# Kernel tuning notes

Hardware: AMD Instinct MI355X
Metric: run time of the kernel (lower is better)

## Reference

```python
import jax, jax.numpy as jnp
import numpy as np

SEQ = 8192
D_IN = 1024
D_OUT = 128


def setup_inputs() -> dict:
    key = jax.random.key(0)
    k0, k1, k2, k3 = jax.random.split(key, 4)
    # kaiming-normal-ish init for weights (std = sqrt(2/fan_in))
    std = np.sqrt(2.0 / D_IN).astype(np.float32)
    return {
        "x": jax.random.normal(k0, (SEQ, D_IN), dtype=jnp.float32),
        "wq": jax.random.normal(k1, (D_IN, D_OUT), dtype=jnp.float32) * std,
        "wk": jax.random.normal(k2, (D_IN, D_OUT), dtype=jnp.float32) * std,
        "wv": jax.random.normal(k3, (D_IN, D_OUT), dtype=jnp.float32) * std,
    }


def reference(x, wq, wk, wv):
    # q,k,v: [S, d_out]
    q = x @ wq
    k = x @ wk
    v = x @ wv
    scale = jnp.sqrt(jnp.asarray(D_OUT, dtype=q.dtype))
    scores = (q @ k.T) / scale          # [S, S]
    attn = jax.nn.softmax(scores, axis=-1)
    return attn @ v                      # [S, d_out]
```

## Files before the change

kernel.cpp:

```cpp
#include <hip/hip_runtime.h>
#include <cstdint>

#define SEQ    8192
#define DIN    1024
#define DOUT   128
#define NSPLIT 8
#define KVTILE 64
#define QTILE  128
#define QK_SCALE 0.1275174246f
#define RESCALE_THR 8.0f

typedef unsigned short u16;
typedef __bf16 bf16x8 __attribute__((ext_vector_type(8)));
typedef float  f32x4  __attribute__((ext_vector_type(4)));
typedef float  f32x16 __attribute__((ext_vector_type(16)));
typedef unsigned short u16x8 __attribute__((ext_vector_type(8)));
typedef unsigned short u16x4 __attribute__((ext_vector_type(4)));

__device__ __forceinline__ u16 bfc(float f) {
  return __builtin_bit_cast(u16, (__bf16)f);
}
__device__ __forceinline__ float bf2f(u16 u) {
  union { uint32_t u; float f; } c; c.u = ((uint32_t)u) << 16; return c.f;
}

__device__ __forceinline__ bf16x8 ldsu8(const u16* base, int byteoff) {
  return __builtin_bit_cast(bf16x8,
    *reinterpret_cast<const u16x8*>(reinterpret_cast<const char*>(base) + byteoff));
}
__device__ __forceinline__ bf16x8 glbu8(const u16* p) {
  return __builtin_bit_cast(bf16x8, *reinterpret_cast<const u16x8*>(p));
}

__device__ __forceinline__ void gload_lds16(const void* g, void* l) {
  __builtin_amdgcn_global_load_lds(
      (const __attribute__((address_space(1))) void*)g,
      (__attribute__((address_space(3))) void*)l, 16, 0, 0);
}

__global__ __launch_bounds__(256) void k_wtrans(const float* __restrict__ wq,
                                                const float* __restrict__ wk,
                                                const float* __restrict__ wv,
                                                u16* __restrict__ Wt) {
  const float* w = (blockIdx.y == 0) ? wq : (blockIdx.y == 1) ? wk : wv;
  int idx = blockIdx.x * 256 + threadIdx.x;
  int k = idx >> 7, n = idx & 127;
  Wt[(size_t)blockIdx.y * (DOUT * DIN) + (size_t)n * DIN + k] = bfc(w[idx]);
}

__global__ __launch_bounds__(256) void k_xcast(const float* __restrict__ x,
                                               u16* __restrict__ Xb) {
  size_t base = ((size_t)blockIdx.x * 256 + threadIdx.x) * 8;
  float4 lo = *reinterpret_cast<const float4*>(x + base);
  float4 hi = *reinterpret_cast<const float4*>(x + base + 4);
  u16x8 v = { bfc(lo.x), bfc(lo.y), bfc(lo.z), bfc(lo.w),
              bfc(hi.x), bfc(hi.y), bfc(hi.z), bfc(hi.w) };
  *reinterpret_cast<u16x8*>(Xb + base) = v;
}

__global__ __launch_bounds__(256, 2) void k_gemm(const u16* __restrict__ Xb,
                                                 const u16* __restrict__ Wt,
                                                 u16* __restrict__ Q,
                                                 u16* __restrict__ K,
                                                 u16* __restrict__ Vt) {
  __shared__ __attribute__((aligned(16))) u16 As[2][64 * 128];
  __shared__ __attribute__((aligned(16))) u16 Bs[2][96 * 128];
  const int tid  = threadIdx.x;
  const int lane = tid & 63, wave = tid >> 6;
  const int lm   = lane & 15, g = lane >> 4;
  const int wm   = wave >> 1, wn = wave & 1;
  const int m0   = blockIdx.x * 64;
  const int n0   = blockIdx.y * 96;
  const int swzr = (lm & 7) << 4;

  const int trow = tid >> 4;
  const int tswz = ((tid & 15) << 4) ^ ((trow & 7) << 4);
  const char* baseA = (const char*)Xb + (size_t)(m0 + trow) * 2048 + tswz;
  const char* baseB = (const char*)Wt + (size_t)(n0 + trow) * 2048 + tswz;

  auto stage = [&](int buf, int kc) {
    const int kb = kc * 256;
#pragma unroll
    for (int i = 0; i < 4; ++i)
      gload_lds16(baseA + kb + i * 32768, &As[buf][i * 2048 + wave * 512]);
#pragma unroll
    for (int j = 0; j < 6; ++j)
      gload_lds16(baseB + kb + j * 32768, &Bs[buf][j * 2048 + wave * 512]);
  };

  f32x4 acc[2][3];
#pragma unroll
  for (int s = 0; s < 2; ++s)
#pragma unroll
    for (int nb = 0; nb < 3; ++nb) acc[s][nb] = (f32x4){0.f, 0.f, 0.f, 0.f};

  auto compute = [&](int buf) {
    const u16* As_ = As[buf];
    const u16* Bs_ = Bs[buf];
    bf16x8 a[2][4], b[3][4];
#pragma unroll
    for (int s = 0; s < 2; ++s)
#pragma unroll
      for (int t = 0; t < 4; ++t)
        a[s][t] = ldsu8(As_, (wm * 32 + s * 16 + lm) * 256 +
                             ((t * 64 + 16 * g) ^ swzr));
#pragma unroll
    for (int nb = 0; nb < 3; ++nb)
#pragma unroll
      for (int t = 0; t < 4; ++t)
        b[nb][t] = ldsu8(Bs_, (wn * 48 + nb * 16 + lm) * 256 +
                              ((t * 64 + 16 * g) ^ swzr));
#pragma unroll
    for (int s = 0; s < 2; ++s)
#pragma unroll
      for (int nb = 0; nb < 3; ++nb)
#pragma unroll
        for (int t = 0; t < 4; ++t)
          acc[s][nb] = __builtin_amdgcn_mfma_f32_16x16x32_bf16(
              a[s][t], b[nb][t], acc[s][nb], 0, 0, 0);
  };

  stage(0, 0);
  asm volatile("s_waitcnt vmcnt(0)" ::: "memory");
  __syncthreads();

#pragma unroll
  for (int kc = 0; kc < 8; kc += 2) {
    if (kc + 1 < 8) stage(1, kc + 1);
    compute(0);
    asm volatile("s_waitcnt vmcnt(0)" ::: "memory");
    __syncthreads();
    if (kc + 2 < 8) stage(0, kc + 2);
    compute(1);
    asm volatile("s_waitcnt vmcnt(0)" ::: "memory");
    __syncthreads();
  }

#pragma unroll
  for (int s = 0; s < 2; ++s)
#pragma unroll
    for (int nb = 0; nb < 3; ++nb) {
      int n = n0 + wn * 48 + nb * 16 + lm;
      int which = n >> 7, col = n & 127;
#pragma unroll
      for (int r = 0; r < 4; ++r) {
        int m = m0 + wm * 32 + s * 16 + g * 4 + r;
        if (which == 0)       Q[(size_t)m * DOUT + col] = bfc(acc[s][nb][r] * QK_SCALE);
        else if (which == 1)  K[(size_t)m * DOUT + col] = bfc(acc[s][nb][r]);
        else                  Vt[(size_t)col * SEQ + m] = bfc(acc[s][nb][r]);
      }
    }
}

__global__ __launch_bounds__(256, 2) void k_attn(const u16* __restrict__ Q,
                                                 const u16* __restrict__ K,
                                                 const u16* __restrict__ Vt,
                                                 u16* __restrict__ Op,
                                                 float* __restrict__ Mb,
                                                 float* __restrict__ Lb) {
  __shared__ __attribute__((aligned(16))) u16 Ks[2][64 * 128];
  __shared__ __attribute__((aligned(16))) u16 Vts[2][128 * 64];
  __shared__ __attribute__((aligned(16))) u16 Ps[4][32 * 64];
  const int tid  = threadIdx.x;
  const int lane = tid & 63, wave = tid >> 6;
  const int l31  = lane & 31, h = lane >> 5;
  const int bid  = blockIdx.x;
  const int split = bid & 7;
  const int m0   = (bid >> 3) * QTILE;
  const int kvbase = split * (SEQ / NSPLIT);
  const int NIT = (SEQ / NSPLIT) / KVTILE;

  auto stage = [&](int buf, int kv0) {
#pragma unroll
    for (int i = 0; i < 4; ++i) {
      int krow = wave * 16 + i * 4 + (lane >> 4);
      const char* gk = (const char*)K + ((size_t)(kv0 + krow) << 8) +
                       (((lane & 15) << 4) ^ ((krow & 7) << 4));
      gload_lds16(gk, &Ks[buf][wave * 2048 + i * 512]);
      int vrow = wave * 32 + i * 8 + (lane >> 3);
      const char* gv = (const char*)Vt + (size_t)vrow * (SEQ * 2) +
                       (size_t)kv0 * 2 +
                       (((lane & 7) << 4) ^ ((vrow & 7) << 4));
      gload_lds16(gv, &Vts[buf][wave * 2048 + i * 512]);
    }
  };

  bf16x8 qf[8];
  stage(0, kvbase);
  {
    const u16* qp = Q + (size_t)(m0 + wave * 32 + l31) * DOUT + 8 * h;
#pragma unroll
    for (int t = 0; t < 8; ++t) qf[t] = glbu8(qp + t * 16);
  }
  asm volatile("s_waitcnt vmcnt(0)" ::: "memory");
  __syncthreads();

  f32x16 o[4] = {};
  float mr = -1e30f, lr = 0.f;

  u16* pw = Ps[wave];
  char* pwb = reinterpret_cast<char*>(pw) + l31 * 128;
  const int pswz = (l31 & 7) << 4;
  int cur = 0;

  for (int it = 0; it < NIT; ++it) {
    if (it + 1 < NIT) stage(cur ^ 1, kvbase + (it + 1) * KVTILE);

    const u16* ks = Ks[cur];
    const u16* vs = Vts[cur];

    f32x16 s[2];
    __builtin_amdgcn_s_setprio(1);
#pragma unroll
    for (int kb = 0; kb < 2; ++kb) {
      f32x16 a = {};
      int krow = kb * 32 + l31;
      int rswz = (krow & 7) << 4;
#pragma unroll
      for (int t = 0; t < 8; ++t) {
        bf16x8 kf = ldsu8(ks, krow * 256 + ((t * 32 + 16 * h) ^ rswz));
        a = __builtin_amdgcn_mfma_f32_32x32x16_bf16(kf, qf[t], a, 0, 0, 0);
      }
      s[kb] = a;
    }
    __builtin_amdgcn_s_setprio(0);

    float t8[8];
#pragma unroll
    for (int i = 0; i < 8; ++i)
      t8[i] = fmaxf(fmaxf(s[0][2 * i], s[0][2 * i + 1]),
                    fmaxf(s[1][2 * i], s[1][2 * i + 1]));
    float u0 = fmaxf(fmaxf(t8[0], t8[1]), fmaxf(t8[2], t8[3]));
    float u1 = fmaxf(fmaxf(t8[4], t8[5]), fmaxf(t8[6], t8[7]));
    float rm = fmaxf(u0, u1);
    rm = fmaxf(rm, __shfl_xor(rm, 32));

    if (__any(rm - mr > RESCALE_THR)) {
      float mn = fmaxf(mr, rm);
      float alpha = exp2f(mr - mn);
      mr = mn;
      lr *= alpha;
#pragma unroll
      for (int db = 0; db < 4; ++db) o[db] *= alpha;
    }

    float rsum = 0.f;
#pragma unroll
    for (int kb = 0; kb < 2; ++kb)
#pragma unroll
      for (int j = 0; j < 4; ++j) {
        float p0 = exp2f(s[kb][4 * j + 0] - mr);
        float p1 = exp2f(s[kb][4 * j + 1] - mr);
        float p2 = exp2f(s[kb][4 * j + 2] - mr);
        float p3 = exp2f(s[kb][4 * j + 3] - mr);
        u16x4 w = { bfc(p0), bfc(p1), bfc(p2), bfc(p3) };
        *reinterpret_cast<u16x4*>(pwb +
            ((kb * 64 + 16 * j + 8 * h) ^ pswz)) = w;
        rsum += (p0 + p1) + (p2 + p3);
      }
    lr += rsum;

    asm volatile("s_waitcnt lgkmcnt(0)" ::: "memory");
    __builtin_amdgcn_sched_barrier(0);

    __builtin_amdgcn_s_setprio(1);
#pragma unroll
    for (int j = 0; j < 4; ++j) {
      bf16x8 pb = ldsu8(pw, l31 * 128 + ((32 * j + 16 * h) ^ pswz));
#pragma unroll
      for (int db = 0; db < 4; ++db) {
        int vrow = db * 32 + l31;
        bf16x8 vb = ldsu8(vs, vrow * 128 +
                              ((32 * j + 16 * h) ^ ((vrow & 7) << 4)));
        o[db] = __builtin_amdgcn_mfma_f32_32x32x16_bf16(vb, pb, o[db], 0, 0, 0);
      }
    }
    __builtin_amdgcn_s_setprio(0);

    asm volatile("s_waitcnt vmcnt(0)" ::: "memory");
    __syncthreads();
    cur ^= 1;
  }

  lr += __shfl_xor(lr, 32);

  const size_t ob = (size_t)split * SEQ * DOUT;
  const int q = m0 + wave * 32 + l31;
#pragma unroll
  for (int db = 0; db < 4; ++db)
#pragma unroll
    for (int j = 0; j < 4; ++j) {
      u16x4 w = { bfc(o[db][4 * j + 0]), bfc(o[db][4 * j + 1]),
                  bfc(o[db][4 * j + 2]), bfc(o[db][4 * j + 3]) };
      *reinterpret_cast<u16x4*>(Op + ob + (size_t)q * DOUT +
                                db * 32 + 8 * j + 4 * h) = w;
    }
  if (h == 0) {
    Mb[split * SEQ + q] = mr;
    Lb[split * SEQ + q] = lr;
  }
}

__global__ __launch_bounds__(256) void k_combine(const u16* __restrict__ Op,
                                                 const float* __restrict__ Mb,
                                                 const float* __restrict__ Lb,
                                                 float* __restrict__ out) {
  int idx = blockIdx.x * 256 + threadIdx.x;
  int srow = idx >> 7;
  float M = -1e30f;
#pragma unroll
  for (int s = 0; s < NSPLIT; ++s) M = fmaxf(M, Mb[s * SEQ + srow]);
  float num = 0.f, den = 0.f;
  const size_t st = (size_t)SEQ * DOUT;
#pragma unroll
  for (int s = 0; s < NSPLIT; ++s) {
    float e = exp2f(Mb[s * SEQ + srow] - M);
    den += Lb[s * SEQ + srow] * e;
    num += bf2f(Op[s * st + idx]) * e;
  }
  out[idx] = num / den;
}

extern "C" void kernel_launch(void* const* d_in, const int* in_sizes, int n_in,
                              void* d_out, int out_size, void* d_ws, size_t ws_size,
                              hipStream_t stream) {
  const float* x  = (const float*)d_in[0];
  const float* wq = (const float*)d_in[1];
  const float* wk = (const float*)d_in[2];
  const float* wv = (const float*)d_in[3];
  char* ws = (char*)d_ws;

  const size_t MB = (size_t)1 << 20;
  u16*   Wt = (u16*)(ws);
  u16*   Q  = (u16*)(ws + 768 * 1024);
  u16*   K  = (u16*)(ws + 768 * 1024 + 2 * MB);
  u16*   Vt = (u16*)(ws + 768 * 1024 + 4 * MB);
  float* Mb = (float*)(ws + 768 * 1024 + 6 * MB);
  float* Lb = (float*)(ws + 768 * 1024 + 6 * MB + 256 * 1024);
  u16*   Xb = (u16*)(ws + 7 * MB + 256 * 1024);
  u16*   Op = (u16*)(ws + 7 * MB + 256 * 1024);
  float* out = (float*)d_out;

  k_wtrans<<<dim3((DIN * DOUT) / 256, 3), 256, 0, stream>>>(wq, wk, wv, Wt);
  k_xcast<<<dim3((SEQ * DIN) / (256 * 8)), 256, 0, stream>>>(x, Xb);
  k_gemm<<<dim3(SEQ / 64, 4), 256, 0, stream>>>(Xb, Wt, Q, K, Vt);
  k_attn<<<dim3((SEQ / QTILE) * NSPLIT), 256, 0, stream>>>(Q, K, Vt, Op, Mb, Lb);
  k_combine<<<dim3((SEQ * DOUT) / 256), 256, 0, stream>>>(Op, Mb, Lb, out);
}
```

Baseline: 90.91 us.

## Build P operand in registers via permlane32 swap instead of LDS round-trip

Removes the per-wave shared-memory staging of softmax probabilities. The 32x32 MFMA output fragments are rearranged into the B-operand layout with permlane32_swap across the two half-waves. This drops LDS writes, the lgkmcnt wait and the LDS reads of P, and frees shared memory. The exp computation is also interleaved with each PV MFMA chunk, which may improve overlap but changes how instructions are scheduled.

```diff
diff --git a/kernel.cpp b/kernel.cpp
--- a/kernel.cpp
+++ b/kernel.cpp
@@ -16,6 +16,8 @@
 typedef float  f32x16 __attribute__((ext_vector_type(16)));
 typedef unsigned short u16x8 __attribute__((ext_vector_type(8)));
 typedef unsigned short u16x4 __attribute__((ext_vector_type(4)));
+typedef unsigned int u32x2 __attribute__((ext_vector_type(2)));
+typedef unsigned int u32x4 __attribute__((ext_vector_type(4)));
 
 __device__ __forceinline__ u16 bfc(float f) {
   return __builtin_bit_cast(u16, (__bf16)f);
@@ -160,7 +162,6 @@
                                                  float* __restrict__ Lb) {
   __shared__ __attribute__((aligned(16))) u16 Ks[2][64 * 128];
   __shared__ __attribute__((aligned(16))) u16 Vts[2][128 * 64];
-  __shared__ __attribute__((aligned(16))) u16 Ps[4][32 * 64];
   const int tid  = threadIdx.x;
   const int lane = tid & 63, wave = tid >> 6;
   const int l31  = lane & 31, h = lane >> 5;
@@ -198,9 +199,6 @@
   f32x16 o[4] = {};
   float mr = -1e30f, lr = 0.f;
 
-  u16* pw = Ps[wave];
-  char* pwb = reinterpret_cast<char*>(pw) + l31 * 128;
-  const int pswz = (l31 & 7) << 4;
   int cur = 0;
 
   for (int it = 0; it < NIT; ++it) {
@@ -246,27 +244,27 @@
 
     float rsum = 0.f;
 #pragma unroll
-    for (int kb = 0; kb < 2; ++kb)
-#pragma unroll
-      for (int j = 0; j < 4; ++j) {
-        float p0 = exp2f(s[kb][4 * j + 0] - mr);
-        float p1 = exp2f(s[kb][4 * j + 1] - mr);
-        float p2 = exp2f(s[kb][4 * j + 2] - mr);
-        float p3 = exp2f(s[kb][4 * j + 3] - mr);
-        u16x4 w = { bfc(p0), bfc(p1), bfc(p2), bfc(p3) };
-        *reinterpret_cast<u16x4*>(pwb +
-            ((kb * 64 + 16 * j + 8 * h) ^ pswz)) = w;
-        rsum += (p0 + p1) + (p2 + p3);
-      }
-    lr += rsum;
-
-    asm volatile("s_waitcnt lgkmcnt(0)" ::: "memory");
-    __builtin_amdgcn_sched_barrier(0);
-
-    __builtin_amdgcn_s_setprio(1);
-#pragma unroll
     for (int j = 0; j < 4; ++j) {
-      bf16x8 pb = ldsu8(pw, l31 * 128 + ((32 * j + 16 * h) ^ pswz));
+      const int kb = j >> 1;
+      const int base = (j & 1) * 8;
+      float e0 = exp2f(s[kb][base + 0] - mr);
+      float e1 = exp2f(s[kb][base + 1] - mr);
+      float e2 = exp2f(s[kb][base + 2] - mr);
+      float e3 = exp2f(s[kb][base + 3] - mr);
+      float e4 = exp2f(s[kb][base + 4] - mr);
+      float e5 = exp2f(s[kb][base + 5] - mr);
+      float e6 = exp2f(s[kb][base + 6] - mr);
+      float e7 = exp2f(s[kb][base + 7] - mr);
+      rsum += ((e0 + e1) + (e2 + e3)) + ((e4 + e5) + (e6 + e7));
+      u16x4 wa = { bfc(e0), bfc(e1), bfc(e2), bfc(e3) };
+      u16x4 wb = { bfc(e4), bfc(e5), bfc(e6), bfc(e7) };
+      u32x2 A = __builtin_bit_cast(u32x2, wa);
+      u32x2 B = __builtin_bit_cast(u32x2, wb);
+      u32x2 r01 = __builtin_amdgcn_permlane32_swap(A.x, B.x, false, false);
+      u32x2 r23 = __builtin_amdgcn_permlane32_swap(A.y, B.y, false, false);
+      u32x4 fr = { r01.x, r23.x, r01.y, r23.y };
+      bf16x8 pb = __builtin_bit_cast(bf16x8, fr);
+      __builtin_amdgcn_s_setprio(1);
 #pragma unroll
       for (int db = 0; db < 4; ++db) {
         int vrow = db * 32 + l31;
@@ -274,8 +272,9 @@
                               ((32 * j + 16 * h) ^ ((vrow & 7) << 4)));
         o[db] = __builtin_amdgcn_mfma_f32_32x32x16_bf16(vb, pb, o[db], 0, 0, 0);
       }
-    }
-    __builtin_amdgcn_s_setprio(0);
+      __builtin_amdgcn_s_setprio(0);
+    }
+    lr += rsum;
 
     asm volatile("s_waitcnt vmcnt(0)" ::: "memory");
     __syncthreads();
```

New measurement: 89.88 us. No clear change (-1.1%).
